# Kernel optimization log

Measured on AMD Instinct MI355X. Metric: run time of the kernel, lower is better.

Reference implementation:

```python
import jax, jax.numpy as jnp
import numpy as np

B, SQ, SK, D, DV = 8, 2048, 4096, 512, 256

def setup_inputs() -> dict:
    key = jax.random.key(0)
    k1, k2, k3, k4, k5 = jax.random.split(key, 5)
    X = jax.random.normal(k1, (B, SQ, D), dtype=jnp.float32)
    Y = jax.random.normal(k2, (SK, D), dtype=jnp.float32)
    Z = jax.random.normal(k3, (SK, D), dtype=jnp.float32)
    # Linear weights (torch stores [out, in]); scaled like default init
    W_k = jax.random.normal(k4, (D, D), dtype=jnp.float32) / np.sqrt(D)
    W_v = jax.random.normal(k5, (DV, D), dtype=jnp.float32) / np.sqrt(D)
    return {"X": X, "Y": Y, "Z": Z, "W_k": W_k, "W_v": W_v, "rate": 0}


def reference(X, Y, Z, W_k, W_v, rate):
    # key = W_k(Y).unsqueeze(0): [1, SK, D]; value = W_v(Z).unsqueeze(0): [1, SK, DV]
    key = (Y @ W_k.T)[None]
    value = (Z @ W_v.T)[None]
    # scores = X @ key^T / sqrt(d): [B, SQ, SK] (key batch dim broadcasts)
    scale = 1.0 / jnp.sqrt(jnp.asarray(X.shape[-1], dtype=X.dtype))
    scores = jnp.matmul(X, jnp.swapaxes(key, 1, 2)) * scale
    attn = jax.nn.softmax(scores, axis=-1)
    # dropout layers act as identity in eval mode
    out = jnp.matmul(attn, value)  # [B, SQ, DV]
    return out
```

## Files before the change

### kernel.cpp

```cpp
#include <hip/hip_runtime.h>
#include <hip/hip_bf16.h>

#define NB    8
#define SQN   2048
#define SKN   4096
#define DDIM  512
#define DVDIM 256
#define NROWS (NB*SQN)
#define NS    2
#define NJ    ((SKN/64)/NS)

typedef __attribute__((ext_vector_type(8)))  short bf16x8;
typedef __attribute__((ext_vector_type(4)))  short bf16x4;
typedef __attribute__((ext_vector_type(4)))  float f32x4;
typedef __attribute__((ext_vector_type(16))) float f32x16;

__device__ __forceinline__ short f2bf(float f) {
    unsigned u = __float_as_uint(f);
    return (short)((u + 0x7FFFu + ((u >> 16) & 1u)) >> 16);
}

#define BAR_LGKM() do {                                                       \
    asm volatile("s_waitcnt lgkmcnt(0)" ::: "memory");                        \
    __builtin_amdgcn_sched_barrier(0);                                        \
    __builtin_amdgcn_s_barrier();                                             \
    __builtin_amdgcn_sched_barrier(0);                                        \
} while (0)

__global__ __launch_bounds__(256, 2) void proj_gemms(
    const float* __restrict__ Y, const float* __restrict__ Z,
    const float* __restrict__ Wk, const float* __restrict__ Wv,
    unsigned short* __restrict__ keyb, unsigned short* __restrict__ vtb)
{
    __shared__ short sA[64*128];
    __shared__ short sB[64*128];
    const float *A, *Bm;
    unsigned short* C;
    int m0, n0;
    const bool kpath = (blockIdx.z == 0);
    if (kpath) {
        A = Y; Bm = Wk; C = keyb;
        m0 = blockIdx.x * 64; n0 = blockIdx.y * 64;
    } else {
        int lin = blockIdx.x * 8 + blockIdx.y;
        if (lin >= 256) return;
        A = Wv; Bm = Z; C = vtb;
        m0 = (lin >> 6) * 64; n0 = (lin & 63) * 64;
    }
    const int tid  = threadIdx.x;
    const int wave = tid >> 6;
    const int lane = tid & 63;
    const int quad = lane >> 4;
    const int l15  = lane & 15;

    f32x4 acc[4];
    #pragma unroll
    for (int n = 0; n < 4; ++n) { acc[n][0]=0.f; acc[n][1]=0.f; acc[n][2]=0.f; acc[n][3]=0.f; }

    float4 ra[8], rb[8];
    #pragma unroll
    for (int it = 0; it < 8; ++it) {
        int f = it*1024 + tid*4, row = f >> 7, col = f & 127;
        ra[it] = *(const float4*)(A  + (size_t)(m0+row)*DDIM + col);
        rb[it] = *(const float4*)(Bm + (size_t)(n0+row)*DDIM + col);
    }

    for (int kc = 0; kc < DDIM; kc += 128) {
        __syncthreads();
        #pragma unroll
        for (int it = 0; it < 8; ++it) {
            int f = it*1024 + tid*4;
            bf16x4 a4; a4[0]=f2bf(ra[it].x); a4[1]=f2bf(ra[it].y); a4[2]=f2bf(ra[it].z); a4[3]=f2bf(ra[it].w);
            *(bf16x4*)(sA + f) = a4;
            bf16x4 b4; b4[0]=f2bf(rb[it].x); b4[1]=f2bf(rb[it].y); b4[2]=f2bf(rb[it].z); b4[3]=f2bf(rb[it].w);
            *(bf16x4*)(sB + f) = b4;
        }
        __syncthreads();
        if (kc + 128 < DDIM) {
            #pragma unroll
            for (int it = 0; it < 8; ++it) {
                int f = it*1024 + tid*4, row = f >> 7, col = f & 127;
                ra[it] = *(const float4*)(A  + (size_t)(m0+row)*DDIM + kc + 128 + col);
                rb[it] = *(const float4*)(Bm + (size_t)(n0+row)*DDIM + kc + 128 + col);
            }
        }
        #pragma unroll
        for (int t = 0; t < 4; ++t) {
            bf16x8 af = *(const bf16x8*)(sA + (wave*16 + l15)*128 + t*32 + quad*8);
            #pragma unroll
            for (int n = 0; n < 4; ++n) {
                bf16x8 bfr = *(const bf16x8*)(sB + (n*16 + l15)*128 + t*32 + quad*8);
                acc[n] = __builtin_amdgcn_mfma_f32_16x16x32_bf16(af, bfr, acc[n], 0, 0, 0);
            }
        }
    }
    #pragma unroll
    for (int n = 0; n < 4; ++n)
        #pragma unroll
        for (int r = 0; r < 4; ++r) {
            int m  = m0 + wave*16 + quad*4 + r;
            int nn = n0 + n*16 + l15;
            unsigned short v = (unsigned short)f2bf(acc[n][r]);
            size_t off;
            if (kpath) {
                int J = m >> 6, kh = (m >> 5) & 1, ls = m & 31;
                int c = nn >> 7, tp = (nn >> 4) & 7, hd = (nn >> 3) & 1, d7 = nn & 7;
                off = (size_t)(((J*4 + c)*8 + tp)*2 + kh)*512 + (hd*32 + ls)*8 + d7;
            } else {
                int J = nn >> 6, g = (nn >> 4) & 3, hk = (nn >> 3) & 1, k7 = nn & 7;
                int wv = m >> 7, n2 = (m >> 5) & 3, lv = m & 31;
                off = (size_t)((J*8 + wv*4 + n2)*4 + g)*512 + (hk*32 + lv)*8 + k7;
            }
            C[off] = v;
        }
}

__global__ __launch_bounds__(128, 1) void attn_fused(
    const float* __restrict__ X,
    const unsigned short* __restrict__ Kb,
    const unsigned short* __restrict__ Vt,
    float* __restrict__ Opart,
    float* __restrict__ Mpart,
    float* __restrict__ Lpart)
{
    __shared__ __align__(16) char smem[74752];
    char* sQ   = smem;
    char* sPex = smem + 65536;
    float* sSt = (float*)(smem + 73728);

    const int tid  = threadIdx.x;
    const int wk   = tid >> 6;
    const int lane = tid & 63;
    const int l31  = lane & 31;
    const int hi   = lane >> 5;

    const int bid   = blockIdx.x;
    const int xcd   = bid & 7;
    const int slot  = bid >> 3;
    const int split = xcd >> 2;
    const int q0    = ((xcd & 3)*64 + slot) * 64;
    const float scale = 0.04419417382415922f * 1.4426950408889634f;

    {
        const float* xrow = X + (size_t)(q0 + wk*32 + l31)*DDIM + hi*8;
        char* qst = sQ + wk*32768;
        #pragma unroll
        for (int t2 = 0; t2 < 32; ++t2) {
            float4 a = *(const float4*)(xrow + t2*16);
            float4 b = *(const float4*)(xrow + t2*16 + 4);
            bf16x8 q;
            q[0]=f2bf(a.x*scale); q[1]=f2bf(a.y*scale); q[2]=f2bf(a.z*scale); q[3]=f2bf(a.w*scale);
            q[4]=f2bf(b.x*scale); q[5]=f2bf(b.y*scale); q[6]=f2bf(b.z*scale); q[7]=f2bf(b.w*scale);
            *(bf16x8*)(qst + t2*1024 + lane*16) = q;
        }
    }

    f32x16 o[2][4];
    #pragma unroll
    for (int g2 = 0; g2 < 2; ++g2)
        #pragma unroll
        for (int n = 0; n < 4; ++n)
            #pragma unroll
            for (int r = 0; r < 16; ++r) o[g2][n][r] = 0.f;
    float m_r[2] = {-1e30f, -1e30f};
    float l_r[2] = {0.f, 0.f};

    const int Jg0 = split * NJ;
    const char* kp = (const char*)Kb + (size_t)Jg0*65536 + wk*1024 + lane*16;
    const char* vp = (const char*)Vt + (size_t)Jg0*32768 + wk*16384 + lane*16;
    #define KOFF(h_, t_) ((size_t)((h_)>>1)*16384 + (size_t)((((h_)&1)*4 + (t_))*2)*1024)

    bf16x8 kf[3][4];
    bf16x8 vf[4][4];

    BAR_LGKM();

    #pragma unroll
    for (int t = 0; t < 4; ++t) kf[0][t] = *(const bf16x8*)(kp + KOFF(0, t));
    #pragma unroll
    for (int t = 0; t < 4; ++t) kf[1][t] = *(const bf16x8*)(kp + KOFF(1, t));

    const char* qb = sQ + lane*16;

    for (int j = 0; j < NJ; ++j) {
        f32x16 s[2];
        #pragma unroll
        for (int g2 = 0; g2 < 2; ++g2)
            #pragma unroll
            for (int r = 0; r < 16; ++r) s[g2][r] = 0.f;

        #pragma unroll
        for (int h = 0; h < 8; ++h) {
            if (h < 6) {
                #pragma unroll
                for (int t = 0; t < 4; ++t)
                    kf[(h + 2) % 3][t] = *(const bf16x8*)(kp + KOFF(h + 2, t));
            } else {
                #pragma unroll
                for (int gg = 0; gg < 2; ++gg) {
                    const int g = (h - 6)*2 + gg;
                    #pragma unroll
                    for (int n = 0; n < 4; ++n)
                        vf[g][n] = *(const bf16x8*)(vp + n*4096 + g*1024);
                }
            }
            __builtin_amdgcn_s_setprio(1);
            #pragma unroll
            for (int t = 0; t < 4; ++t) {
                #pragma unroll
                for (int g2 = 0; g2 < 2; ++g2) {
                    bf16x8 qv = *(const bf16x8*)(qb + g2*32768 + (h*4 + t)*1024);
                    s[g2] = __builtin_amdgcn_mfma_f32_32x32x16_bf16(
                            kf[h % 3][t], qv, s[g2], 0, 0, 0);
                }
            }
            __builtin_amdgcn_s_setprio(0);
        }

        float tmax[2];
        #pragma unroll
        for (int g2 = 0; g2 < 2; ++g2) {
            float v = fmaxf(fmaxf(fmaxf(s[g2][0],s[g2][1]),fmaxf(s[g2][2],s[g2][3])),
                            fmaxf(fmaxf(s[g2][4],s[g2][5]),fmaxf(s[g2][6],s[g2][7])));
            v = fmaxf(v, fmaxf(fmaxf(fmaxf(s[g2][8],s[g2][9]),fmaxf(s[g2][10],s[g2][11])),
                               fmaxf(fmaxf(s[g2][12],s[g2][13]),fmaxf(s[g2][14],s[g2][15]))));
            v = fmaxf(v, __shfl_xor(v, 32));
            tmax[g2] = v;
            if (lane < 32) sSt[((wk*2 + g2)*2 + 0)*32 + lane] = v;
        }
        BAR_LGKM();
        bool  upd[2]; float mn[2], tsum[2];
        #pragma unroll
        for (int g2 = 0; g2 < 2; ++g2) {
            float tmax_o = sSt[(((wk^1)*2 + g2)*2 + 0)*32 + l31];
            float tj = fmaxf(tmax[g2], tmax_o);
            upd[g2] = tj > m_r[g2] + 8.0f;
            mn[g2]  = upd[g2] ? tj : m_r[g2];
            float ts = 0.f;
            #pragma unroll
            for (int r = 0; r < 16; ++r) {
                float pv = exp2f(s[g2][r] - mn[g2]); s[g2][r] = pv; ts += pv;
            }
            ts += __shfl_xor(ts, 32);
            tsum[g2] = ts;
        }

        bf16x8 pf[2][2];
        #pragma unroll
        for (int g2 = 0; g2 < 2; ++g2)
            #pragma unroll
            for (int ks = 0; ks < 2; ++ks) {
                int wA, wB, wC, wD;
                asm("v_cvt_pk_bf16_f32 %0, %1, %2" : "=v"(wA) : "v"(s[g2][8*ks+0]), "v"(s[g2][8*ks+1]));
                asm("v_cvt_pk_bf16_f32 %0, %1, %2" : "=v"(wB) : "v"(s[g2][8*ks+2]), "v"(s[g2][8*ks+3]));
                asm("v_cvt_pk_bf16_f32 %0, %1, %2" : "=v"(wC) : "v"(s[g2][8*ks+4]), "v"(s[g2][8*ks+5]));
                asm("v_cvt_pk_bf16_f32 %0, %1, %2" : "=v"(wD) : "v"(s[g2][8*ks+6]), "v"(s[g2][8*ks+7]));
                asm("v_permlane32_swap_b32 %0, %1" : "+v"(wA), "+v"(wC));
                asm("v_permlane32_swap_b32 %0, %1" : "+v"(wB), "+v"(wD));
                union { int w[4]; bf16x8 v; } u;
                u.w[0] = wA; u.w[1] = wB; u.w[2] = wC; u.w[3] = wD;
                pf[g2][ks] = u.v;
                *(bf16x8*)(sPex + (g2*4 + wk*2 + ks)*1024 + lane*16) = u.v;
            }
        #pragma unroll
        for (int g2 = 0; g2 < 2; ++g2)
            if (lane < 32) sSt[((wk*2 + g2)*2 + 1)*32 + lane] = tsum[g2];

        if (j + 1 < NJ) {
            kp += 65536;
            #pragma unroll
            for (int t = 0; t < 4; ++t) kf[0][t] = *(const bf16x8*)(kp + KOFF(0, t));
            #pragma unroll
            for (int t = 0; t < 4; ++t) kf[1][t] = *(const bf16x8*)(kp + KOFF(1, t));
        }
        BAR_LGKM();
        int any_upd = 0;
        #pragma unroll
        for (int g2 = 0; g2 < 2; ++g2) {
            float tsum_o = sSt[(((wk^1)*2 + g2)*2 + 1)*32 + l31];
            float alpha  = upd[g2] ? exp2f(m_r[g2] - mn[g2]) : 1.0f;
            l_r[g2] = l_r[g2]*alpha + (tsum[g2] + tsum_o);
            m_r[g2] = mn[g2];
            any_upd |= (int)upd[g2];
            if (__any(upd[g2])) {
                #pragma unroll
                for (int r = 0; r < 16; ++r) {
                    int row = (r&3) + 8*(r>>2) + 4*hi;
                    float ar = __shfl(alpha, row);
                    #pragma unroll
                    for (int n = 0; n < 4; ++n) o[g2][n][r] *= ar;
                }
            }
        }

        const char* pb = sPex + lane*16;
        __builtin_amdgcn_s_setprio(1);
        #pragma unroll
        for (int g = 0; g < 4; ++g) {
            bf16x8 pa0 = ((g >> 1) == wk) ? pf[0][g & 1]
                        : *(const bf16x8*)(pb + (0*4 + g)*1024);
            bf16x8 pa1 = ((g >> 1) == wk) ? pf[1][g & 1]
                        : *(const bf16x8*)(pb + (1*4 + g)*1024);
            #pragma unroll
            for (int n = 0; n < 4; ++n) {
                o[0][n] = __builtin_amdgcn_mfma_f32_32x32x16_bf16(
                        pa0, vf[g][n], o[0][n], 0, 0, 0);
                o[1][n] = __builtin_amdgcn_mfma_f32_32x32x16_bf16(
                        pa1, vf[g][n], o[1][n], 0, 0, 0);
            }
        }
        __builtin_amdgcn_s_setprio(0);
        vp += 32768;
    }
    #undef KOFF

    const size_t base = (size_t)split * NROWS;
    #pragma unroll
    for (int g2 = 0; g2 < 2; ++g2) {
        const int gr0 = q0 + g2*32;
        if (wk == 0 && lane < 32) {
            Mpart[base + gr0 + lane] = m_r[g2];
            Lpart[base + gr0 + lane] = l_r[g2];
        }
        #pragma unroll
        for (int r = 0; r < 16; ++r) {
            int row = (r&3) + 8*(r>>2) + 4*hi;
            float* orow = Opart + (base + gr0 + row) * (size_t)DVDIM + wk*128;
            #pragma unroll
            for (int n = 0; n < 4; ++n)
                orow[n*32 + l31] = o[g2][n][r];
        }
    }
}

__global__ void combine_splits(
    const float* __restrict__ Opart, const float* __restrict__ Mpart,
    const float* __restrict__ Lpart, float* __restrict__ out)
{
    const int row = blockIdx.x * 4 + (threadIdx.x >> 6);
    const int dv4 = (threadIdx.x & 63) * 4;
    float M = -1e30f;
    #pragma unroll
    for (int s = 0; s < NS; ++s) M = fmaxf(M, Mpart[(size_t)s*NROWS + row]);
    float denom = 0.f;
    float4 acc = make_float4(0.f, 0.f, 0.f, 0.f);
    #pragma unroll
    for (int s = 0; s < NS; ++s) {
        float w = exp2f(Mpart[(size_t)s*NROWS + row] - M);
        denom += Lpart[(size_t)s*NROWS + row] * w;
        float4 ov = *(const float4*)(Opart + ((size_t)s*NROWS + row)*DVDIM + dv4);
        acc.x += ov.x*w; acc.y += ov.y*w; acc.z += ov.z*w; acc.w += ov.w*w;
    }
    float inv = 1.0f / denom;
    *(float4*)(out + (size_t)row*DVDIM + dv4)
        = make_float4(acc.x*inv, acc.y*inv, acc.z*inv, acc.w*inv);
}

extern "C" void kernel_launch(void* const* d_in, const int* in_sizes, int n_in,
                              void* d_out, int out_size, void* d_ws, size_t ws_size,
                              hipStream_t stream) {
    const float* X  = (const float*)d_in[0];
    const float* Y  = (const float*)d_in[1];
    const float* Z  = (const float*)d_in[2];
    const float* Wk = (const float*)d_in[3];
    const float* Wv = (const float*)d_in[4];
    float* out = (float*)d_out;

    char* ws = (char*)d_ws;
    unsigned short* keyb = (unsigned short*)ws;
    unsigned short* vtb  = (unsigned short*)(ws + (4u<<20));
    float* Opart = (float*)(ws + (6u<<20));
    float* Mpart = (float*)(ws + (6u<<20) + (size_t)NS*NROWS*DVDIM*4);
    float* Lpart = Mpart + (size_t)NS*NROWS;

    proj_gemms<<<dim3(64, 8, 2), dim3(256), 0, stream>>>(Y, Z, Wk, Wv, keyb, vtb);
    attn_fused<<<dim3(512), dim3(128), 0, stream>>>(
        X, keyb, vtb, Opart, Mpart, Lpart);
    combine_splits<<<dim3(NROWS/4), dim3(256), 0, stream>>>(Opart, Mpart, Lpart, out);
}
```

Baseline: 249.8 us.

## Software-pipeline next tile's QK^T MFMAs across current tile's softmax and PV

Restructures the attention loop so the QK^T score MFMAs for the next key tile are interleaved with the current tile's softmax reductions, barriers and PV MFMAs, using two ping-ponged score accumulators (sA_/sB_) and a loop unrolled by two. The intent is to hide the cross-wave LDS barrier waits and the exp/convert work behind matrix-core work. It adds a second 32-float accumulator set per wave, which raises register pressure and may lower occupancy or cause spills. The V loads are also pulled earlier, into the tail of the next tile's QK phase.

```diff
diff --git a/kernel.cpp b/kernel.cpp
--- a/kernel.cpp
+++ b/kernel.cpp
@@ -172,146 +172,178 @@
 
     bf16x8 kf[3][4];
     bf16x8 vf[4][4];
+    f32x16 sA_[2], sB_[2];
 
     BAR_LGKM();
 
-    #pragma unroll
-    for (int t = 0; t < 4; ++t) kf[0][t] = *(const bf16x8*)(kp + KOFF(0, t));
-    #pragma unroll
-    for (int t = 0; t < 4; ++t) kf[1][t] = *(const bf16x8*)(kp + KOFF(1, t));
+    #define LD_KF(buf_, h_)                                                   \
+        do { _Pragma("unroll")                                                \
+             for (int t_ = 0; t_ < 4; ++t_)                                   \
+                 kf[buf_][t_] = *(const bf16x8*)(kp + KOFF(h_, t_));          \
+        } while (0)
+
+    #define LD_V(half_, voff_)                                                \
+        do { _Pragma("unroll")                                                \
+             for (int gg_ = 0; gg_ < 2; ++gg_)                                \
+                 _Pragma("unroll")                                            \
+                 for (int n_ = 0; n_ < 4; ++n_)                               \
+                     vf[(half_)*2 + gg_][n_] = *(const bf16x8*)(vp + (voff_)  \
+                         + n_*4096 + ((half_)*2 + gg_)*1024);                 \
+        } while (0)
 
     const char* qb = sQ + lane*16;
 
-    for (int j = 0; j < NJ; ++j) {
-        f32x16 s[2];
-        #pragma unroll
-        for (int g2 = 0; g2 < 2; ++g2)
-            #pragma unroll
-            for (int r = 0; r < 16; ++r) s[g2][r] = 0.f;
-
-        #pragma unroll
-        for (int h = 0; h < 8; ++h) {
-            if (h < 6) {
-                #pragma unroll
-                for (int t = 0; t < 4; ++t)
-                    kf[(h + 2) % 3][t] = *(const bf16x8*)(kp + KOFF(h + 2, t));
-            } else {
-                #pragma unroll
-                for (int gg = 0; gg < 2; ++gg) {
-                    const int g = (h - 6)*2 + gg;
-                    #pragma unroll
-                    for (int n = 0; n < 4; ++n)
-                        vf[g][n] = *(const bf16x8*)(vp + n*4096 + g*1024);
-                }
-            }
-            __builtin_amdgcn_s_setprio(1);
-            #pragma unroll
-            for (int t = 0; t < 4; ++t) {
-                #pragma unroll
-                for (int g2 = 0; g2 < 2; ++g2) {
-                    bf16x8 qv = *(const bf16x8*)(qb + g2*32768 + (h*4 + t)*1024);
-                    s[g2] = __builtin_amdgcn_mfma_f32_32x32x16_bf16(
-                            kf[h % 3][t], qv, s[g2], 0, 0, 0);
-                }
-            }
-            __builtin_amdgcn_s_setprio(0);
-        }
-
-        float tmax[2];
-        #pragma unroll
-        for (int g2 = 0; g2 < 2; ++g2) {
-            float v = fmaxf(fmaxf(fmaxf(s[g2][0],s[g2][1]),fmaxf(s[g2][2],s[g2][3])),
-                            fmaxf(fmaxf(s[g2][4],s[g2][5]),fmaxf(s[g2][6],s[g2][7])));
-            v = fmaxf(v, fmaxf(fmaxf(fmaxf(s[g2][8],s[g2][9]),fmaxf(s[g2][10],s[g2][11])),
-                               fmaxf(fmaxf(s[g2][12],s[g2][13]),fmaxf(s[g2][14],s[g2][15]))));
-            v = fmaxf(v, __shfl_xor(v, 32));
-            tmax[g2] = v;
-            if (lane < 32) sSt[((wk*2 + g2)*2 + 0)*32 + lane] = v;
-        }
-        BAR_LGKM();
-        bool  upd[2]; float mn[2], tsum[2];
-        #pragma unroll
-        for (int g2 = 0; g2 < 2; ++g2) {
-            float tmax_o = sSt[(((wk^1)*2 + g2)*2 + 0)*32 + l31];
-            float tj = fmaxf(tmax[g2], tmax_o);
-            upd[g2] = tj > m_r[g2] + 8.0f;
-            mn[g2]  = upd[g2] ? tj : m_r[g2];
-            float ts = 0.f;
-            #pragma unroll
-            for (int r = 0; r < 16; ++r) {
-                float pv = exp2f(s[g2][r] - mn[g2]); s[g2][r] = pv; ts += pv;
-            }
-            ts += __shfl_xor(ts, 32);
-            tsum[g2] = ts;
-        }
-
-        bf16x8 pf[2][2];
-        #pragma unroll
-        for (int g2 = 0; g2 < 2; ++g2)
-            #pragma unroll
-            for (int ks = 0; ks < 2; ++ks) {
-                int wA, wB, wC, wD;
-                asm("v_cvt_pk_bf16_f32 %0, %1, %2" : "=v"(wA) : "v"(s[g2][8*ks+0]), "v"(s[g2][8*ks+1]));
-                asm("v_cvt_pk_bf16_f32 %0, %1, %2" : "=v"(wB) : "v"(s[g2][8*ks+2]), "v"(s[g2][8*ks+3]));
-                asm("v_cvt_pk_bf16_f32 %0, %1, %2" : "=v"(wC) : "v"(s[g2][8*ks+4]), "v"(s[g2][8*ks+5]));
-                asm("v_cvt_pk_bf16_f32 %0, %1, %2" : "=v"(wD) : "v"(s[g2][8*ks+6]), "v"(s[g2][8*ks+7]));
-                asm("v_permlane32_swap_b32 %0, %1" : "+v"(wA), "+v"(wC));
-                asm("v_permlane32_swap_b32 %0, %1" : "+v"(wB), "+v"(wD));
-                union { int w[4]; bf16x8 v; } u;
-                u.w[0] = wA; u.w[1] = wB; u.w[2] = wC; u.w[3] = wD;
-                pf[g2][ks] = u.v;
-                *(bf16x8*)(sPex + (g2*4 + wk*2 + ks)*1024 + lane*16) = u.v;
-            }
-        #pragma unroll
-        for (int g2 = 0; g2 < 2; ++g2)
-            if (lane < 32) sSt[((wk*2 + g2)*2 + 1)*32 + lane] = tsum[g2];
-
-        if (j + 1 < NJ) {
-            kp += 65536;
-            #pragma unroll
-            for (int t = 0; t < 4; ++t) kf[0][t] = *(const bf16x8*)(kp + KOFF(0, t));
-            #pragma unroll
-            for (int t = 0; t < 4; ++t) kf[1][t] = *(const bf16x8*)(kp + KOFF(1, t));
-        }
-        BAR_LGKM();
-        int any_upd = 0;
-        #pragma unroll
-        for (int g2 = 0; g2 < 2; ++g2) {
-            float tsum_o = sSt[(((wk^1)*2 + g2)*2 + 1)*32 + l31];
-            float alpha  = upd[g2] ? exp2f(m_r[g2] - mn[g2]) : 1.0f;
-            l_r[g2] = l_r[g2]*alpha + (tsum[g2] + tsum_o);
-            m_r[g2] = mn[g2];
-            any_upd |= (int)upd[g2];
-            if (__any(upd[g2])) {
-                #pragma unroll
-                for (int r = 0; r < 16; ++r) {
-                    int row = (r&3) + 8*(r>>2) + 4*hi;
-                    float ar = __shfl(alpha, row);
-                    #pragma unroll
-                    for (int n = 0; n < 4; ++n) o[g2][n][r] *= ar;
-                }
-            }
-        }
-
-        const char* pb = sPex + lane*16;
-        __builtin_amdgcn_s_setprio(1);
-        #pragma unroll
-        for (int g = 0; g < 4; ++g) {
-            bf16x8 pa0 = ((g >> 1) == wk) ? pf[0][g & 1]
-                        : *(const bf16x8*)(pb + (0*4 + g)*1024);
-            bf16x8 pa1 = ((g >> 1) == wk) ? pf[1][g & 1]
-                        : *(const bf16x8*)(pb + (1*4 + g)*1024);
-            #pragma unroll
-            for (int n = 0; n < 4; ++n) {
-                o[0][n] = __builtin_amdgcn_mfma_f32_32x32x16_bf16(
-                        pa0, vf[g][n], o[0][n], 0, 0, 0);
-                o[1][n] = __builtin_amdgcn_mfma_f32_32x32x16_bf16(
-                        pa1, vf[g][n], o[1][n], 0, 0, 0);
-            }
-        }
-        __builtin_amdgcn_s_setprio(0);
-        vp += 32768;
-    }
+    #define QK_PH(SN_, buf_, h_)                                              \
+        do {                                                                  \
+            __builtin_amdgcn_s_setprio(1);                                    \
+            _Pragma("unroll")                                                 \
+            for (int t_ = 0; t_ < 4; ++t_) {                                  \
+                bf16x8 q0_ = *(const bf16x8*)(qb + ((h_)*4 + t_)*1024);       \
+                bf16x8 q1_ = *(const bf16x8*)(qb + 32768 + ((h_)*4 + t_)*1024);\
+                SN_[0] = __builtin_amdgcn_mfma_f32_32x32x16_bf16(             \
+                            kf[buf_][t_], q0_, SN_[0], 0, 0, 0);              \
+                SN_[1] = __builtin_amdgcn_mfma_f32_32x32x16_bf16(             \
+                            kf[buf_][t_], q1_, SN_[1], 0, 0, 0);              \
+            }                                                                 \
+            __builtin_amdgcn_s_setprio(0);                                    \
+        } while (0)
+
+    LD_KF(0, 0); LD_KF(1, 1);
+    #pragma unroll
+    for (int g2 = 0; g2 < 2; ++g2)
+        #pragma unroll
+        for (int r = 0; r < 16; ++r) sA_[g2][r] = 0.f;
+    LD_KF(2, 2); QK_PH(sA_, 0, 0);
+    LD_KF(0, 3); QK_PH(sA_, 1, 1);
+    LD_KF(1, 4); QK_PH(sA_, 2, 2);
+    LD_KF(2, 5); QK_PH(sA_, 0, 3);
+    LD_KF(0, 6); QK_PH(sA_, 1, 4);
+    LD_KF(1, 7); QK_PH(sA_, 2, 5);
+    LD_V(0, 0);  QK_PH(sA_, 0, 6);
+    LD_V(1, 0);  QK_PH(sA_, 1, 7);
+    kp += 65536;
+    LD_KF(0, 0); LD_KF(1, 1);
+
+    #define ITER(jv, SC, SN)                                                  \
+    {                                                                         \
+        const bool hasN = (jv) + 1 < NJ;                                      \
+                                   \
+        float tmx[2];                                                         \
+        _Pragma("unroll")                                                     \
+        for (int g2 = 0; g2 < 2; ++g2) {                                      \
+            float v = fmaxf(fmaxf(fmaxf(SC[g2][0],SC[g2][1]),fmaxf(SC[g2][2],SC[g2][3])), \
+                            fmaxf(fmaxf(SC[g2][4],SC[g2][5]),fmaxf(SC[g2][6],SC[g2][7]))); \
+            v = fmaxf(v, fmaxf(fmaxf(fmaxf(SC[g2][8],SC[g2][9]),fmaxf(SC[g2][10],SC[g2][11])), \
+                               fmaxf(fmaxf(SC[g2][12],SC[g2][13]),fmaxf(SC[g2][14],SC[g2][15])))); \
+            v = fmaxf(v, __shfl_xor(v, 32));                                  \
+            tmx[g2] = v;                                                      \
+            if (lane < 32) sSt[((wk*2 + g2)*2 + 0)*32 + lane] = v;            \
+        }                                                                     \
+                        \
+        if (hasN) {                                                           \
+            _Pragma("unroll")                                                 \
+            for (int g2 = 0; g2 < 2; ++g2)                                    \
+                _Pragma("unroll")                                             \
+                for (int r = 0; r < 16; ++r) SN[g2][r] = 0.f;                 \
+            LD_KF(2, 2); QK_PH(SN, 0, 0);                                     \
+            LD_KF(0, 3); QK_PH(SN, 1, 1);                                     \
+            LD_KF(1, 4); QK_PH(SN, 2, 2);                                     \
+            LD_KF(2, 5); QK_PH(SN, 0, 3);                                     \
+        }                                                                     \
+        BAR_LGKM();                                           \
+                                 \
+        bool upd[2]; float mn[2], tsum[2], alpha[2];                          \
+        bf16x8 pf[2][2];                                                      \
+        _Pragma("unroll")                                                     \
+        for (int g2 = 0; g2 < 2; ++g2) {                                      \
+            float to = sSt[(((wk^1)*2 + g2)*2 + 0)*32 + l31];                 \
+            float tj = fmaxf(tmx[g2], to);                                    \
+            upd[g2] = tj > m_r[g2] + 8.0f;                 \
+            mn[g2]  = upd[g2] ? tj : m_r[g2];                                 \
+            alpha[g2] = upd[g2] ? exp2f(m_r[g2] - mn[g2]) : 1.0f;             \
+            float ts = 0.f;                                                   \
+            _Pragma("unroll")                                                 \
+            for (int r = 0; r < 16; ++r) {                                    \
+                float pv = exp2f(SC[g2][r] - mn[g2]); SC[g2][r] = pv; ts += pv; \
+            }                                                                 \
+            ts += __shfl_xor(ts, 32);                                         \
+            tsum[g2] = ts;                                                    \
+            if (lane < 32) sSt[((wk*2 + g2)*2 + 1)*32 + lane] = ts;           \
+            _Pragma("unroll")                                                 \
+            for (int ks = 0; ks < 2; ++ks) {                                  \
+                int wA, wB, wC, wD;                                           \
+                asm("v_cvt_pk_bf16_f32 %0, %1, %2" : "=v"(wA) : "v"(SC[g2][8*ks+0]), "v"(SC[g2][8*ks+1])); \
+                asm("v_cvt_pk_bf16_f32 %0, %1, %2" : "=v"(wB) : "v"(SC[g2][8*ks+2]), "v"(SC[g2][8*ks+3])); \
+                asm("v_cvt_pk_bf16_f32 %0, %1, %2" : "=v"(wC) : "v"(SC[g2][8*ks+4]), "v"(SC[g2][8*ks+5])); \
+                asm("v_cvt_pk_bf16_f32 %0, %1, %2" : "=v"(wD) : "v"(SC[g2][8*ks+6]), "v"(SC[g2][8*ks+7])); \
+                asm("v_permlane32_swap_b32 %0, %1" : "+v"(wA), "+v"(wC));     \
+                asm("v_permlane32_swap_b32 %0, %1" : "+v"(wB), "+v"(wD));     \
+                union { int w[4]; bf16x8 v; } u;                              \
+                u.w[0] = wA; u.w[1] = wB; u.w[2] = wC; u.w[3] = wD;           \
+                pf[g2][ks] = u.v;                                             \
+                *(bf16x8*)(sPex + (g2*4 + wk*2 + ks)*1024 + lane*16) = u.v;   \
+            }                                                                 \
+        }                                                                     \
+                               \
+        if (hasN) {                                                           \
+            LD_KF(0, 6); QK_PH(SN, 1, 4);                                     \
+            LD_KF(1, 7); QK_PH(SN, 2, 5);                                     \
+        }                                                                     \
+        BAR_LGKM();                                           \
+                      \
+        _Pragma("unroll")                                                     \
+        for (int g2 = 0; g2 < 2; ++g2) {                                      \
+            float tso = sSt[(((wk^1)*2 + g2)*2 + 1)*32 + l31];                \
+            l_r[g2] = l_r[g2]*alpha[g2] + (tsum[g2] + tso);                   \
+            m_r[g2] = mn[g2];                                                 \
+            if (__any(upd[g2])) {                                             \
+                _Pragma("unroll")                                             \
+                for (int r = 0; r < 16; ++r) {                                \
+                    int row = (r&3) + 8*(r>>2) + 4*hi;                        \
+                    float ar = __shfl(alpha[g2], row);                        \
+                    _Pragma("unroll")                                         \
+                    for (int n = 0; n < 4; ++n) o[g2][n][r] *= ar;            \
+                }                                                             \
+            }                                                                 \
+        }                                                                     \
+         \
+        {                                                                     \
+            const char* pb_ = sPex + lane*16;                                 \
+            __builtin_amdgcn_s_setprio(1);                                    \
+            _Pragma("unroll")                                                 \
+            for (int g = 0; g < 4; ++g) {                                     \
+                bf16x8 pa0 = ((g >> 1) == wk) ? pf[0][g & 1]                  \
+                            : *(const bf16x8*)(pb_ + (0*4 + g)*1024);         \
+                bf16x8 pa1 = ((g >> 1) == wk) ? pf[1][g & 1]                  \
+                            : *(const bf16x8*)(pb_ + (1*4 + g)*1024);         \
+                _Pragma("unroll")                                             \
+                for (int n = 0; n < 4; ++n) {                                 \
+                    o[0][n] = __builtin_amdgcn_mfma_f32_32x32x16_bf16(        \
+                            pa0, vf[g][n], o[0][n], 0, 0, 0);                 \
+                    o[1][n] = __builtin_amdgcn_mfma_f32_32x32x16_bf16(        \
+                            pa1, vf[g][n], o[1][n], 0, 0, 0);                 \
+                }                                                             \
+            }                                                                 \
+            __builtin_amdgcn_s_setprio(0);                                    \
+        }                                                                     \
+                \
+        if (hasN) {                                                           \
+            LD_V(0, 32768); QK_PH(SN, 0, 6);                                  \
+            LD_V(1, 32768); QK_PH(SN, 1, 7);                                  \
+            kp += 65536;                                                      \
+            if ((jv) + 2 < NJ) { LD_KF(0, 0); LD_KF(1, 1); }                  \
+        }                                                                     \
+        vp += 32768;                                                          \
+    }
+
+    for (int j = 0; j < NJ; j += 2) {
+        ITER(j,     sA_, sB_);
+        ITER(j + 1, sB_, sA_);
+    }
+    #undef ITER
+    #undef QK_PH
+    #undef LD_V
+    #undef LD_KF
     #undef KOFF
 
     const size_t base = (size_t)split * NROWS;
```

Result: slower. 275.9 us (+10.4%).
